# Optimization experiments

Measured on AMD Instinct MI355X. Metric: run time of the kernel, lower is better.

## Reference

```python
import jax, jax.numpy as jnp
import numpy as np

D = 1024      # in_features
H = 768       # hidden_features per routed expert
E = 8         # n_routed_experts
K = 2         # n_activated_experts
NS = 2        # n_shared_experts
ROUTE_SCALE = 1.0


def setup_inputs() -> dict:
    key = jax.random.key(0)
    ks = jax.random.split(key, 6)
    s = 0.02
    return {
        "x": jax.random.normal(ks[0], (2, 1024, D), jnp.float32),
        "gate_w": jax.random.normal(ks[1], (E, D), jnp.float32) * s,
        "W1": jax.random.normal(ks[2], (E, 2 * H, D), jnp.float32) * s,   # expert fc1 (y|gate)
        "W2": jax.random.normal(ks[3], (E, D, H), jnp.float32) * s,       # expert fc2
        "Ws1": jax.random.normal(ks[4], (2 * NS * H, D), jnp.float32) * s,  # shared fc1
        "Ws2": jax.random.normal(ks[5], (D, NS * H), jnp.float32) * s,      # shared fc2
    }


def _gated_mlp(x, w1, w2):
    # GatedMLP: fc1 -> chunk(2) -> y * silu(gate) -> fc2, all bias-free
    h = x @ w1.T
    y, g = jnp.split(h, 2, axis=-1)
    return (y * jax.nn.silu(g)) @ w2.T


def reference(x, gate_w, W1, W2, Ws1, Ws2):
    x_shape = x.shape
    xf = x.reshape(-1, D)                 # [T, D]
    T = xf.shape[0]

    # --- Gate: softmax scores in fp32, top-k routing ---
    scores = jax.nn.softmax((xf @ gate_w.T).astype(jnp.float32), axis=-1)  # [T, E]
    top_vals, top_idx = jax.lax.top_k(scores, K)
    # no bias branch (in_features != 7168): gathered original scores == top_k values
    weights = (top_vals * ROUTE_SCALE).astype(x.dtype)                      # [T, K]

    # Dense per-token/expert combine weights (0 for unselected experts);
    # mathematically identical to the per-expert gather/scatter-add combine.
    w_dense = jnp.zeros((T, E), x.dtype).at[jnp.arange(T)[:, None], top_idx].set(weights)

    # --- Routed experts (stacked GatedMLPs) ---
    h = jnp.einsum('td,ehd->teh', xf, W1)        # [T, E, 2H]
    y, g = jnp.split(h, 2, axis=-1)
    eo = jnp.einsum('teh,edh->ted', y * jax.nn.silu(g), W2)  # [T, E, D]
    z = jnp.einsum('te,ted->td', w_dense, eo)    # weighted combine

    # --- Shared experts ---
    z = z + _gated_mlp(xf, Ws1, Ws2)
    return z.reshape(x_shape)
```

## Files before the change

### kernel.cpp

```cpp
#include <hip/hip_runtime.h>
#include <hip/hip_bf16.h>


typedef short bf16x8 __attribute__((ext_vector_type(8)));
typedef float f32x4 __attribute__((ext_vector_type(4)));

__device__ __forceinline__ unsigned short f2b(float f) {
    __hip_bfloat16 h = __float2bfloat16(f);
    return *reinterpret_cast<unsigned short*>(&h);
}

__device__ __forceinline__ void ldst16(const unsigned short* g, unsigned short* l) {
    __builtin_amdgcn_global_load_lds(
        (const __attribute__((address_space(1))) unsigned int*)g,
        (__attribute__((address_space(3))) unsigned int*)l, 16, 0, 0);
}

__device__ __forceinline__ void cvt8(const float* s, unsigned short* d, int j) {
    const float4* sp = reinterpret_cast<const float4*>(s) + (size_t)j * 2;
    float4 v0 = sp[0], v1 = sp[1];
    union { unsigned short u[8]; uint4 v; } o;
    o.u[0]=f2b(v0.x); o.u[1]=f2b(v0.y); o.u[2]=f2b(v0.z); o.u[3]=f2b(v0.w);
    o.u[4]=f2b(v1.x); o.u[5]=f2b(v1.y); o.u[6]=f2b(v1.z); o.u[7]=f2b(v1.w);
    *(reinterpret_cast<uint4*>(d) + j) = o.v;
}

__global__ __launch_bounds__(256) void k_convgate(const float* __restrict__ x,
                                                  const float* __restrict__ gw,
                                                  const float* __restrict__ W1,
                                                  const float* __restrict__ Ws1,
                                                  unsigned short* __restrict__ xb,
                                                  unsigned short* __restrict__ W1b,
                                                  unsigned short* __restrict__ Ws1b,
                                                  int* __restrict__ tokslot,
                                                  float* __restrict__ wroute,
                                                  int* __restrict__ cnt,
                                                  float* __restrict__ out) {
    __shared__ float red[4][8];
    __shared__ float sc[8];
    const int b = blockIdx.x, tid = threadIdx.x;
    if (b < 7680) {
        int i = b * 256 + tid;
        if (i < 1572864)  cvt8(W1,  W1b,  i);
        else              cvt8(Ws1, Ws1b, i - 1572864);
        return;
    }
    const int t = b - 7680;
    const int lane = tid & 63, w = tid >> 6;

    float4 v = reinterpret_cast<const float4*>(x + (size_t)t * 1024)[tid];
    union { unsigned short u[4]; ushort4 v4; } o;
    o.u[0]=f2b(v.x); o.u[1]=f2b(v.y); o.u[2]=f2b(v.z); o.u[3]=f2b(v.w);
    reinterpret_cast<ushort4*>(xb + (size_t)t * 1024)[tid] = o.v4;

    float p[8];
    for (int e = 0; e < 8; e++) {
        float4 g = reinterpret_cast<const float4*>(gw + (size_t)e * 1024)[tid];
        p[e] = v.x*g.x + v.y*g.y + v.z*g.z + v.w*g.w;
    }
    for (int e = 0; e < 8; e++)
        for (int off = 32; off > 0; off >>= 1) p[e] += __shfl_down(p[e], off, 64);
    if (lane == 0)
        for (int e = 0; e < 8; e++) red[w][e] = p[e];
    __syncthreads();
    if (tid < 8) sc[tid] = red[0][tid] + red[1][tid] + red[2][tid] + red[3][tid];
    __syncthreads();
    if (tid == 0) {
        float m = sc[0];
        for (int e = 1; e < 8; e++) m = fmaxf(m, sc[e]);
        float ex[8], sum = 0.f;
        for (int e = 0; e < 8; e++) { ex[e] = expf(sc[e] - m); sum += ex[e]; }
        float inv = 1.f / sum;
        int i1 = 0;
        for (int e = 1; e < 8; e++) if (sc[e] > sc[i1]) i1 = e;
        int i2 = -1; float s2 = -1e30f;
        for (int e = 0; e < 8; e++) if (e != i1 && sc[e] > s2) { s2 = sc[e]; i2 = e; }
        int p1 = atomicAdd(&cnt[i1 * 16], 1);
        tokslot[i1 * 2048 + p1] = t; wroute[i1 * 2048 + p1] = ex[i1] * inv;
        int p2 = atomicAdd(&cnt[i2 * 16], 1);
        tokslot[i2 * 2048 + p2] = t; wroute[i2 * 2048 + p2] = ex[i2] * inv;
    }
    reinterpret_cast<float4*>(out + (size_t)t * 1024)[tid] = (float4){0.f, 0.f, 0.f, 0.f};
}

__global__ __launch_bounds__(256) void k_fc1w(const unsigned short* __restrict__ xb,
                                              const unsigned short* __restrict__ W1b,
                                              const unsigned short* __restrict__ Ws1b,
                                              const float* __restrict__ W2,
                                              const float* __restrict__ Ws2,
                                              unsigned short* __restrict__ W2b,
                                              unsigned short* __restrict__ Ws2b,
                                              const int* __restrict__ tokslot,
                                              const float* __restrict__ wroute,
                                              const int* __restrict__ cnt,
                                              unsigned short* __restrict__ act_r,
                                              unsigned short* __restrict__ acts) {
    __shared__ alignas(16) unsigned short As[128 * 64];
    __shared__ alignas(16) unsigned short Bs[128 * 64];
    const int tid = threadIdx.x;
    if (blockIdx.x >= 864) {
        int i = (blockIdx.x - 864) * 256 + tid;
        if (i < 786432)  cvt8(W2,  W2b,  i);
        else             cvt8(Ws2, Ws2b, i - 786432);
        return;
    }
    const int lane = tid & 63, w = tid >> 6;
    const int wr = w >> 1, wc = w & 1;
    const int mt = blockIdx.x / 12, ht = blockIdx.x % 12;

    int pre = 0, sel = -1, base = 0;
    for (int ee = 0; ee < 10; ee++) {
        int til = (ee < 8) ? ((cnt[ee * 16] + 127) >> 7) : 16;
        if (sel < 0 && mt < pre + til) { sel = ee; base = pre; }
        pre += til;
    }
    if (sel < 0) return;
    const int e = sel, m0 = (mt - base) * 128, h0 = ht * 64;
    const int Te = (e < 8) ? cnt[e * 16] : 2048;
    const unsigned short* Bp = (e < 8) ? (W1b + (size_t)e * 1536 * 1024)
                                       : (Ws1b + (size_t)(e - 8) * 768 * 1024);
    const int gOff = (e < 8) ? 768 : 1536;

    const int kc = tid & 7;
    int aoff[4], boff[4];
    for (int q = 0; q < 4; q++) {
        int row = q * 32 + (tid >> 3);
        int idx = m0 + row;
        int tk = (e < 8) ? ((idx < Te) ? tokslot[e * 2048 + idx] : 0) : idx;
        aoff[q] = tk * 1024 + ((kc ^ (row & 7)) << 3);
        int grow = (row < 64) ? (h0 + row) : (gOff + h0 + row - 64);
        boff[q] = grow * 1024 + ((kc ^ (row & 7)) << 3);
    }

    f32x4 accy[4][2], accg[4][2];
    for (int i = 0; i < 4; i++)
        for (int j = 0; j < 2; j++) {
            accy[i][j] = (f32x4){0.f, 0.f, 0.f, 0.f};
            accg[i][j] = (f32x4){0.f, 0.f, 0.f, 0.f};
        }

    for (int k0 = 0; k0 < 1024; k0 += 64) {
        for (int q = 0; q < 4; q++) {
            ldst16(xb + aoff[q] + k0, As + (q * 256 + tid) * 8);
            ldst16(Bp + boff[q] + k0, Bs + (q * 256 + tid) * 8);
        }
        __syncthreads();
        for (int kh = 0; kh < 2; kh++) {
            const int cq = kh * 4 + (lane >> 4);
            bf16x8 a[4], by[2], bg[2];
            for (int i = 0; i < 4; i++) {
                int r = 64 * wr + 16 * i + (lane & 15);
                a[i] = *(const bf16x8*)&As[r * 64 + ((cq ^ (r & 7)) << 3)];
            }
            for (int j = 0; j < 2; j++) {
                int ry = 32 * wc + 16 * j + (lane & 15);
                by[j] = *(const bf16x8*)&Bs[ry * 64 + ((cq ^ (ry & 7)) << 3)];
                int rg = 64 + ry;
                bg[j] = *(const bf16x8*)&Bs[rg * 64 + ((cq ^ (rg & 7)) << 3)];
            }
            __builtin_amdgcn_s_setprio(1);
            for (int i = 0; i < 4; i++)
                for (int j = 0; j < 2; j++) {
                    accy[i][j] = __builtin_amdgcn_mfma_f32_16x16x32_bf16(a[i], by[j], accy[i][j], 0, 0, 0);
                    accg[i][j] = __builtin_amdgcn_mfma_f32_16x16x32_bf16(a[i], bg[j], accg[i][j], 0, 0, 0);
                }
            __builtin_amdgcn_s_setprio(0);
        }
        __syncthreads();
    }

    for (int i = 0; i < 4; i++)
        for (int r = 0; r < 4; r++) {
            int irow = m0 + 64 * wr + 16 * i + ((lane >> 4) << 2) + r;
            if (irow >= Te) continue;
            float sw = (e < 8) ? wroute[e * 2048 + irow] : 1.0f;
            unsigned short* dst = (e < 8)
                ? (act_r + ((size_t)e * 2048 + irow) * 768)
                : (acts + (size_t)irow * 1536 + (size_t)(e - 8) * 768);
            for (int j = 0; j < 2; j++) {
                float y = accy[i][j][r], g = accg[i][j][r];
                float sg = g / (1.0f + __expf(-g));
                int col = h0 + 32 * wc + 16 * j + (lane & 15);
                dst[col] = f2b(sw * y * sg);
            }
        }
}

__global__ __launch_bounds__(256) void k_fc2u(const unsigned short* __restrict__ act_r,
                                              const unsigned short* __restrict__ acts,
                                              const unsigned short* __restrict__ W2b,
                                              const unsigned short* __restrict__ Ws2b,
                                              const int* __restrict__ tokslot,
                                              const int* __restrict__ cnt,
                                              float* __restrict__ out) {
    __shared__ alignas(16) unsigned short As[128 * 128];
    __shared__ alignas(16) unsigned short Bs[64 * 128];
    const int tid = threadIdx.x, lane = tid & 63, w = tid >> 6;
    const int wr = w >> 1, wc = w & 1;
    const int mt = blockIdx.x >> 4, nt = blockIdx.x & 15;

    int pre = 0, sel = -1, base = 0;
    for (int ee = 0; ee < 9; ee++) {
        int til = (ee < 8) ? ((cnt[ee * 16] + 127) >> 7) : 16;
        if (sel < 0 && mt < pre + til) { sel = ee; base = pre; }
        pre += til;
    }
    if (sel < 0) return;
    const int e = sel, m0 = (mt - base) * 128, n0 = nt * 64;
    int Te, astride, bstride, K;
    const unsigned short *Ab, *Bb;
    if (e < 8) {
        Te = cnt[e * 16]; K = 768; astride = 768; bstride = 768;
        Ab = act_r + (size_t)e * 2048 * 768;
        Bb = W2b + (size_t)e * 1024 * 768;
    } else {
        Te = 2048; K = 1536; astride = 1536; bstride = 1536;
        Ab = acts;
        Bb = Ws2b;
    }

    const int cp = tid & 15;
    int aoff[8], boff[4];
    for (int q = 0; q < 8; q++) {
        int row = q * 16 + (tid >> 4);
        aoff[q] = (m0 + row) * astride + ((cp ^ (row & 15)) << 3);
    }
    for (int q = 0; q < 4; q++) {
        int row = q * 16 + (tid >> 4);
        boff[q] = (n0 + row) * bstride + ((cp ^ (row & 15)) << 3);
    }

    f32x4 acc[4][2];
    for (int i = 0; i < 4; i++)
        for (int j = 0; j < 2; j++) acc[i][j] = (f32x4){0.f, 0.f, 0.f, 0.f};

    for (int k0 = 0; k0 < K; k0 += 128) {
        for (int q = 0; q < 8; q++) ldst16(Ab + aoff[q] + k0, As + (q * 256 + tid) * 8);
        for (int q = 0; q < 4; q++) ldst16(Bb + boff[q] + k0, Bs + (q * 256 + tid) * 8);
        __syncthreads();
        for (int kh = 0; kh < 4; kh++) {
            const int cq = kh * 4 + (lane >> 4);
            bf16x8 a[4], b[2];
            for (int i = 0; i < 4; i++) {
                int r = 64 * wr + 16 * i + (lane & 15);
                a[i] = *(const bf16x8*)&As[r * 128 + ((cq ^ (r & 15)) << 3)];
            }
            for (int j = 0; j < 2; j++) {
                int rb = 32 * wc + 16 * j + (lane & 15);
                b[j] = *(const bf16x8*)&Bs[rb * 128 + ((cq ^ (rb & 15)) << 3)];
            }
            __builtin_amdgcn_s_setprio(1);
            for (int i = 0; i < 4; i++)
                for (int j = 0; j < 2; j++)
                    acc[i][j] = __builtin_amdgcn_mfma_f32_16x16x32_bf16(a[i], b[j], acc[i][j], 0, 0, 0);
            __builtin_amdgcn_s_setprio(0);
        }
        __syncthreads();
    }

    for (int i = 0; i < 4; i++)
        for (int r = 0; r < 4; r++) {
            int irow = m0 + 64 * wr + 16 * i + ((lane >> 4) << 2) + r;
            if (irow >= Te) continue;
            int t = (e < 8) ? tokslot[e * 2048 + irow] : irow;
            for (int j = 0; j < 2; j++) {
                int col = n0 + 32 * wc + 16 * j + (lane & 15);
                atomicAdd(out + (size_t)t * 1024 + col, acc[i][j][r]);
            }
        }
}

extern "C" void kernel_launch(void* const* d_in, const int* in_sizes, int n_in,
                              void* d_out, int out_size, void* d_ws, size_t ws_size,
                              hipStream_t stream) {
    const float* x   = (const float*)d_in[0];
    const float* gw  = (const float*)d_in[1];
    const float* W1  = (const float*)d_in[2];
    const float* W2  = (const float*)d_in[3];
    const float* Ws1 = (const float*)d_in[4];
    const float* Ws2 = (const float*)d_in[5];
    float* out = (float*)d_out;

    char* ws = (char*)d_ws;
    unsigned short* xb    = (unsigned short*)(ws + 0);
    unsigned short* W1b   = (unsigned short*)(ws + 4194304);
    unsigned short* Ws1b  = (unsigned short*)(ws + 29360128);
    unsigned short* W2b   = (unsigned short*)(ws + 35651584);
    unsigned short* Ws2b  = (unsigned short*)(ws + 48234496);
    unsigned short* act_r = (unsigned short*)(ws + 51380224);
    unsigned short* acts  = (unsigned short*)(ws + 76546048);
    int*            tokslot = (int*)(ws + 82837504);
    float*          wroute  = (float*)(ws + 82903040);
    int*            cnt     = (int*)(ws + 82968576);

    hipMemsetAsync(cnt, 0, 512, stream);
    k_convgate<<<9728, 256, 0, stream>>>(x, gw, W1, Ws1,
                                         xb, W1b, Ws1b,
                                         tokslot, wroute, cnt, out);
    k_fc1w<<<4704, 256, 0, stream>>>(xb, W1b, Ws1b, W2, Ws2, W2b, Ws2b,
                                     tokslot, wroute, cnt, act_r, acts);
    k_fc2u<<<896, 256, 0, stream>>>(act_r, acts, W2b, Ws2b, tokslot, cnt, out);
}
```

Before: 233.9 us.

## Fuse fc1 and fc2 kernels with per-tile readiness counters

Merges the fc1/activation kernel and the fc2 combine kernel into one launch. fc2 blocks spin on agent-scope atomic ready counters set by the matching fc1 row tiles and by the W2 conversion blocks for their expert. The fc2 K-tile shrinks from 128 to 64 so both phases share one 32KB LDS buffer. This removes a kernel boundary and lets fc2 start while other fc1 tiles are still running, but relies on block scheduling order to avoid deadlock and adds spin-wait cost.

```diff
diff --git a/kernel.cpp b/kernel.cpp
--- a/kernel.cpp
+++ b/kernel.cpp
@@ -83,7 +83,7 @@
     reinterpret_cast<float4*>(out + (size_t)t * 1024)[tid] = (float4){0.f, 0.f, 0.f, 0.f};
 }
 
-__global__ __launch_bounds__(256) void k_fc1w(const unsigned short* __restrict__ xb,
+__global__ __launch_bounds__(256) void k_fc12(const unsigned short* __restrict__ xb,
                                               const unsigned short* __restrict__ W1b,
                                               const unsigned short* __restrict__ Ws1b,
                                               const float* __restrict__ W2,
@@ -92,182 +92,218 @@
                                               unsigned short* __restrict__ Ws2b,
                                               const int* __restrict__ tokslot,
                                               const float* __restrict__ wroute,
-                                              const int* __restrict__ cnt,
+                                              int* __restrict__ cntw,
                                               unsigned short* __restrict__ act_r,
-                                              unsigned short* __restrict__ acts) {
-    __shared__ alignas(16) unsigned short As[128 * 64];
-    __shared__ alignas(16) unsigned short Bs[128 * 64];
-    const int tid = threadIdx.x;
-    if (blockIdx.x >= 864) {
-        int i = (blockIdx.x - 864) * 256 + tid;
+                                              unsigned short* __restrict__ acts,
+                                              float* __restrict__ out) {
+    __shared__ alignas(16) unsigned short smem[16384];
+    const int tid = threadIdx.x, bid = blockIdx.x;
+    int* rdy = cntw + 128;
+    int* cvd = cntw + 128 + 2560;
+
+    if (bid >= 864 && bid < 4704) {
+        const int ci = bid - 864;
+        int i = ci * 256 + tid;
         if (i < 786432)  cvt8(W2,  W2b,  i);
         else             cvt8(Ws2, Ws2b, i - 786432);
+        __syncthreads();
+        if (tid == 0) {
+            int e = (ci < 3072) ? (ci / 384) : 8;
+            __hip_atomic_fetch_add(&cvd[e * 16], 1, __ATOMIC_RELEASE,
+                                   __HIP_MEMORY_SCOPE_AGENT);
+        }
         return;
     }
+
     const int lane = tid & 63, w = tid >> 6;
     const int wr = w >> 1, wc = w & 1;
-    const int mt = blockIdx.x / 12, ht = blockIdx.x % 12;
-
-    int pre = 0, sel = -1, base = 0;
-    for (int ee = 0; ee < 10; ee++) {
-        int til = (ee < 8) ? ((cnt[ee * 16] + 127) >> 7) : 16;
-        if (sel < 0 && mt < pre + til) { sel = ee; base = pre; }
-        pre += til;
-    }
-    if (sel < 0) return;
-    const int e = sel, m0 = (mt - base) * 128, h0 = ht * 64;
-    const int Te = (e < 8) ? cnt[e * 16] : 2048;
-    const unsigned short* Bp = (e < 8) ? (W1b + (size_t)e * 1536 * 1024)
-                                       : (Ws1b + (size_t)(e - 8) * 768 * 1024);
-    const int gOff = (e < 8) ? 768 : 1536;
-
-    const int kc = tid & 7;
-    int aoff[4], boff[4];
-    for (int q = 0; q < 4; q++) {
-        int row = q * 32 + (tid >> 3);
-        int idx = m0 + row;
-        int tk = (e < 8) ? ((idx < Te) ? tokslot[e * 2048 + idx] : 0) : idx;
-        aoff[q] = tk * 1024 + ((kc ^ (row & 7)) << 3);
-        int grow = (row < 64) ? (h0 + row) : (gOff + h0 + row - 64);
-        boff[q] = grow * 1024 + ((kc ^ (row & 7)) << 3);
-    }
-
-    f32x4 accy[4][2], accg[4][2];
-    for (int i = 0; i < 4; i++)
-        for (int j = 0; j < 2; j++) {
-            accy[i][j] = (f32x4){0.f, 0.f, 0.f, 0.f};
-            accg[i][j] = (f32x4){0.f, 0.f, 0.f, 0.f};
-        }
-
-    for (int k0 = 0; k0 < 1024; k0 += 64) {
+
+    if (bid < 864) {
+        unsigned short* As = smem;
+        unsigned short* Bs = smem + 8192;
+        const int mt = bid / 12, ht = bid % 12;
+
+        int pre = 0, sel = -1, base = 0;
+        for (int ee = 0; ee < 10; ee++) {
+            int til = (ee < 8) ? ((cntw[ee * 16] + 127) >> 7) : 16;
+            if (sel < 0 && mt < pre + til) { sel = ee; base = pre; }
+            pre += til;
+        }
+        if (sel < 0) return;
+        const int e = sel, m0 = (mt - base) * 128, h0 = ht * 64, mtl = mt - base;
+        const int Te = (e < 8) ? cntw[e * 16] : 2048;
+        const unsigned short* Bp = (e < 8) ? (W1b + (size_t)e * 1536 * 1024)
+                                           : (Ws1b + (size_t)(e - 8) * 768 * 1024);
+        const int gOff = (e < 8) ? 768 : 1536;
+
+        const int kc = tid & 7;
+        int aoff[4], boff[4];
         for (int q = 0; q < 4; q++) {
-            ldst16(xb + aoff[q] + k0, As + (q * 256 + tid) * 8);
-            ldst16(Bp + boff[q] + k0, Bs + (q * 256 + tid) * 8);
-        }
+            int row = q * 32 + (tid >> 3);
+            int idx = m0 + row;
+            int tk = (e < 8) ? ((idx < Te) ? tokslot[e * 2048 + idx] : 0) : idx;
+            aoff[q] = tk * 1024 + ((kc ^ (row & 7)) << 3);
+            int grow = (row < 64) ? (h0 + row) : (gOff + h0 + row - 64);
+            boff[q] = grow * 1024 + ((kc ^ (row & 7)) << 3);
+        }
+
+        f32x4 accy[4][2], accg[4][2];
+        for (int i = 0; i < 4; i++)
+            for (int j = 0; j < 2; j++) {
+                accy[i][j] = (f32x4){0.f, 0.f, 0.f, 0.f};
+                accg[i][j] = (f32x4){0.f, 0.f, 0.f, 0.f};
+            }
+
+        for (int k0 = 0; k0 < 1024; k0 += 64) {
+            for (int q = 0; q < 4; q++) {
+                ldst16(xb + aoff[q] + k0, As + (q * 256 + tid) * 8);
+                ldst16(Bp + boff[q] + k0, Bs + (q * 256 + tid) * 8);
+            }
+            __syncthreads();
+            for (int kh = 0; kh < 2; kh++) {
+                const int cq = kh * 4 + (lane >> 4);
+                bf16x8 a[4], by[2], bg[2];
+                for (int i = 0; i < 4; i++) {
+                    int r = 64 * wr + 16 * i + (lane & 15);
+                    a[i] = *(const bf16x8*)&As[r * 64 + ((cq ^ (r & 7)) << 3)];
+                }
+                for (int j = 0; j < 2; j++) {
+                    int ry = 32 * wc + 16 * j + (lane & 15);
+                    by[j] = *(const bf16x8*)&Bs[ry * 64 + ((cq ^ (ry & 7)) << 3)];
+                    int rg = 64 + ry;
+                    bg[j] = *(const bf16x8*)&Bs[rg * 64 + ((cq ^ (rg & 7)) << 3)];
+                }
+                __builtin_amdgcn_s_setprio(1);
+                for (int i = 0; i < 4; i++)
+                    for (int j = 0; j < 2; j++) {
+                        accy[i][j] = __builtin_amdgcn_mfma_f32_16x16x32_bf16(a[i], by[j], accy[i][j], 0, 0, 0);
+                        accg[i][j] = __builtin_amdgcn_mfma_f32_16x16x32_bf16(a[i], bg[j], accg[i][j], 0, 0, 0);
+                    }
+                __builtin_amdgcn_s_setprio(0);
+            }
+            __syncthreads();
+        }
+
+        for (int i = 0; i < 4; i++)
+            for (int r = 0; r < 4; r++) {
+                int irow = m0 + 64 * wr + 16 * i + ((lane >> 4) << 2) + r;
+                if (irow >= Te) continue;
+                float sw = (e < 8) ? wroute[e * 2048 + irow] : 1.0f;
+                unsigned short* dst = (e < 8)
+                    ? (act_r + ((size_t)e * 2048 + irow) * 768)
+                    : (acts + (size_t)irow * 1536 + (size_t)(e - 8) * 768);
+                for (int j = 0; j < 2; j++) {
+                    float y = accy[i][j][r], g = accg[i][j][r];
+                    float sg = g / (1.0f + __expf(-g));
+                    int col = h0 + 32 * wc + 16 * j + (lane & 15);
+                    dst[col] = f2b(sw * y * sg);
+                }
+            }
         __syncthreads();
-        for (int kh = 0; kh < 2; kh++) {
-            const int cq = kh * 4 + (lane >> 4);
-            bf16x8 a[4], by[2], bg[2];
-            for (int i = 0; i < 4; i++) {
-                int r = 64 * wr + 16 * i + (lane & 15);
-                a[i] = *(const bf16x8*)&As[r * 64 + ((cq ^ (r & 7)) << 3)];
-            }
-            for (int j = 0; j < 2; j++) {
-                int ry = 32 * wc + 16 * j + (lane & 15);
-                by[j] = *(const bf16x8*)&Bs[ry * 64 + ((cq ^ (ry & 7)) << 3)];
-                int rg = 64 + ry;
-                bg[j] = *(const bf16x8*)&Bs[rg * 64 + ((cq ^ (rg & 7)) << 3)];
-            }
-            __builtin_amdgcn_s_setprio(1);
-            for (int i = 0; i < 4; i++)
+        if (tid == 0)
+            __hip_atomic_fetch_add(&rdy[(e * 16 + mtl) * 16], 1, __ATOMIC_RELEASE,
+                                   __HIP_MEMORY_SCOPE_AGENT);
+        return;
+    }
+
+    {
+        unsigned short* As = smem;
+        unsigned short* Bs = smem + 8192;
+        const int fb = bid - 4704;
+        const int mt = fb >> 4, nt = fb & 15;
+
+        int pre = 0, sel = -1, base = 0;
+        for (int ee = 0; ee < 9; ee++) {
+            int til = (ee < 8) ? ((cntw[ee * 16] + 127) >> 7) : 16;
+            if (sel < 0 && mt < pre + til) { sel = ee; base = pre; }
+            pre += til;
+        }
+        if (sel < 0) return;
+        const int e = sel, m0 = (mt - base) * 128, n0 = nt * 64, mtl = mt - base;
+        int Te, astride, bstride, K;
+        const unsigned short *Ab, *Bb;
+        if (e < 8) {
+            Te = cntw[e * 16]; K = 768; astride = 768; bstride = 768;
+            Ab = act_r + (size_t)e * 2048 * 768;
+            Bb = W2b + (size_t)e * 1024 * 768;
+        } else {
+            Te = 2048; K = 1536; astride = 1536; bstride = 1536;
+            Ab = acts;
+            Bb = Ws2b;
+        }
+
+        if (tid == 0) {
+            int spins = 0;
+            if (e < 8) {
+                while (__hip_atomic_load(&rdy[(e * 16 + mtl) * 16], __ATOMIC_ACQUIRE,
+                                         __HIP_MEMORY_SCOPE_AGENT) < 12
+                       && spins < (1 << 22)) { __builtin_amdgcn_s_sleep(8); spins++; }
+                while (__hip_atomic_load(&cvd[e * 16], __ATOMIC_ACQUIRE,
+                                         __HIP_MEMORY_SCOPE_AGENT) < 384
+                       && spins < (1 << 22)) { __builtin_amdgcn_s_sleep(8); spins++; }
+            } else {
+                while ((__hip_atomic_load(&rdy[(128 + mtl) * 16], __ATOMIC_ACQUIRE,
+                                          __HIP_MEMORY_SCOPE_AGENT) < 12 ||
+                        __hip_atomic_load(&rdy[(144 + mtl) * 16], __ATOMIC_ACQUIRE,
+                                          __HIP_MEMORY_SCOPE_AGENT) < 12)
+                       && spins < (1 << 22)) { __builtin_amdgcn_s_sleep(8); spins++; }
+                while (__hip_atomic_load(&cvd[128], __ATOMIC_ACQUIRE,
+                                         __HIP_MEMORY_SCOPE_AGENT) < 768
+                       && spins < (1 << 22)) { __builtin_amdgcn_s_sleep(8); spins++; }
+            }
+        }
+        __syncthreads();
+
+        const int kc = tid & 7;
+        int aoff[4], boff[2];
+        for (int q = 0; q < 4; q++) {
+            int row = q * 32 + (tid >> 3);
+            aoff[q] = (m0 + row) * astride + ((kc ^ (row & 7)) << 3);
+        }
+        for (int q = 0; q < 2; q++) {
+            int row = q * 32 + (tid >> 3);
+            boff[q] = (n0 + row) * bstride + ((kc ^ (row & 7)) << 3);
+        }
+
+        f32x4 acc[4][2];
+        for (int i = 0; i < 4; i++)
+            for (int j = 0; j < 2; j++) acc[i][j] = (f32x4){0.f, 0.f, 0.f, 0.f};
+
+        for (int k0 = 0; k0 < K; k0 += 64) {
+            for (int q = 0; q < 4; q++) ldst16(Ab + aoff[q] + k0, As + (q * 256 + tid) * 8);
+            for (int q = 0; q < 2; q++) ldst16(Bb + boff[q] + k0, Bs + (q * 256 + tid) * 8);
+            __syncthreads();
+            for (int kh = 0; kh < 2; kh++) {
+                const int cq = kh * 4 + (lane >> 4);
+                bf16x8 a[4], b[2];
+                for (int i = 0; i < 4; i++) {
+                    int r = 64 * wr + 16 * i + (lane & 15);
+                    a[i] = *(const bf16x8*)&As[r * 64 + ((cq ^ (r & 7)) << 3)];
+                }
                 for (int j = 0; j < 2; j++) {
-                    accy[i][j] = __builtin_amdgcn_mfma_f32_16x16x32_bf16(a[i], by[j], accy[i][j], 0, 0, 0);
-                    accg[i][j] = __builtin_amdgcn_mfma_f32_16x16x32_bf16(a[i], bg[j], accg[i][j], 0, 0, 0);
-                }
-            __builtin_amdgcn_s_setprio(0);
-        }
-        __syncthreads();
-    }
-
-    for (int i = 0; i < 4; i++)
-        for (int r = 0; r < 4; r++) {
-            int irow = m0 + 64 * wr + 16 * i + ((lane >> 4) << 2) + r;
-            if (irow >= Te) continue;
-            float sw = (e < 8) ? wroute[e * 2048 + irow] : 1.0f;
-            unsigned short* dst = (e < 8)
-                ? (act_r + ((size_t)e * 2048 + irow) * 768)
-                : (acts + (size_t)irow * 1536 + (size_t)(e - 8) * 768);
-            for (int j = 0; j < 2; j++) {
-                float y = accy[i][j][r], g = accg[i][j][r];
-                float sg = g / (1.0f + __expf(-g));
-                int col = h0 + 32 * wc + 16 * j + (lane & 15);
-                dst[col] = f2b(sw * y * sg);
-            }
-        }
-}
-
-__global__ __launch_bounds__(256) void k_fc2u(const unsigned short* __restrict__ act_r,
-                                              const unsigned short* __restrict__ acts,
-                                              const unsigned short* __restrict__ W2b,
-                                              const unsigned short* __restrict__ Ws2b,
-                                              const int* __restrict__ tokslot,
-                                              const int* __restrict__ cnt,
-                                              float* __restrict__ out) {
-    __shared__ alignas(16) unsigned short As[128 * 128];
-    __shared__ alignas(16) unsigned short Bs[64 * 128];
-    const int tid = threadIdx.x, lane = tid & 63, w = tid >> 6;
-    const int wr = w >> 1, wc = w & 1;
-    const int mt = blockIdx.x >> 4, nt = blockIdx.x & 15;
-
-    int pre = 0, sel = -1, base = 0;
-    for (int ee = 0; ee < 9; ee++) {
-        int til = (ee < 8) ? ((cnt[ee * 16] + 127) >> 7) : 16;
-        if (sel < 0 && mt < pre + til) { sel = ee; base = pre; }
-        pre += til;
-    }
-    if (sel < 0) return;
-    const int e = sel, m0 = (mt - base) * 128, n0 = nt * 64;
-    int Te, astride, bstride, K;
-    const unsigned short *Ab, *Bb;
-    if (e < 8) {
-        Te = cnt[e * 16]; K = 768; astride = 768; bstride = 768;
-        Ab = act_r + (size_t)e * 2048 * 768;
-        Bb = W2b + (size_t)e * 1024 * 768;
-    } else {
-        Te = 2048; K = 1536; astride = 1536; bstride = 1536;
-        Ab = acts;
-        Bb = Ws2b;
-    }
-
-    const int cp = tid & 15;
-    int aoff[8], boff[4];
-    for (int q = 0; q < 8; q++) {
-        int row = q * 16 + (tid >> 4);
-        aoff[q] = (m0 + row) * astride + ((cp ^ (row & 15)) << 3);
-    }
-    for (int q = 0; q < 4; q++) {
-        int row = q * 16 + (tid >> 4);
-        boff[q] = (n0 + row) * bstride + ((cp ^ (row & 15)) << 3);
-    }
-
-    f32x4 acc[4][2];
-    for (int i = 0; i < 4; i++)
-        for (int j = 0; j < 2; j++) acc[i][j] = (f32x4){0.f, 0.f, 0.f, 0.f};
-
-    for (int k0 = 0; k0 < K; k0 += 128) {
-        for (int q = 0; q < 8; q++) ldst16(Ab + aoff[q] + k0, As + (q * 256 + tid) * 8);
-        for (int q = 0; q < 4; q++) ldst16(Bb + boff[q] + k0, Bs + (q * 256 + tid) * 8);
-        __syncthreads();
-        for (int kh = 0; kh < 4; kh++) {
-            const int cq = kh * 4 + (lane >> 4);
-            bf16x8 a[4], b[2];
-            for (int i = 0; i < 4; i++) {
-                int r = 64 * wr + 16 * i + (lane & 15);
-                a[i] = *(const bf16x8*)&As[r * 128 + ((cq ^ (r & 15)) << 3)];
-            }
-            for (int j = 0; j < 2; j++) {
-                int rb = 32 * wc + 16 * j + (lane & 15);
-                b[j] = *(const bf16x8*)&Bs[rb * 128 + ((cq ^ (rb & 15)) << 3)];
-            }
-            __builtin_amdgcn_s_setprio(1);
-            for (int i = 0; i < 4; i++)
-                for (int j = 0; j < 2; j++)
-                    acc[i][j] = __builtin_amdgcn_mfma_f32_16x16x32_bf16(a[i], b[j], acc[i][j], 0, 0, 0);
-            __builtin_amdgcn_s_setprio(0);
-        }
-        __syncthreads();
-    }
-
-    for (int i = 0; i < 4; i++)
-        for (int r = 0; r < 4; r++) {
-            int irow = m0 + 64 * wr + 16 * i + ((lane >> 4) << 2) + r;
-            if (irow >= Te) continue;
-            int t = (e < 8) ? tokslot[e * 2048 + irow] : irow;
-            for (int j = 0; j < 2; j++) {
-                int col = n0 + 32 * wc + 16 * j + (lane & 15);
-                atomicAdd(out + (size_t)t * 1024 + col, acc[i][j][r]);
-            }
-        }
+                    int rb = 32 * wc + 16 * j + (lane & 15);
+                    b[j] = *(const bf16x8*)&Bs[rb * 64 + ((cq ^ (rb & 7)) << 3)];
+                }
+                __builtin_amdgcn_s_setprio(1);
+                for (int i = 0; i < 4; i++)
+                    for (int j = 0; j < 2; j++)
+                        acc[i][j] = __builtin_amdgcn_mfma_f32_16x16x32_bf16(a[i], b[j], acc[i][j], 0, 0, 0);
+                __builtin_amdgcn_s_setprio(0);
+            }
+            __syncthreads();
+        }
+
+        for (int i = 0; i < 4; i++)
+            for (int r = 0; r < 4; r++) {
+                int irow = m0 + 64 * wr + 16 * i + ((lane >> 4) << 2) + r;
+                if (irow >= Te) continue;
+                int t = (e < 8) ? tokslot[e * 2048 + irow] : irow;
+                for (int j = 0; j < 2; j++) {
+                    int col = n0 + 32 * wc + 16 * j + (lane & 15);
+                    atomicAdd(out + (size_t)t * 1024 + col, acc[i][j][r]);
+                }
+            }
+    }
 }
 
 extern "C" void kernel_launch(void* const* d_in, const int* in_sizes, int n_in,
@@ -293,11 +329,10 @@
     float*          wroute  = (float*)(ws + 82903040);
     int*            cnt     = (int*)(ws + 82968576);
 
-    hipMemsetAsync(cnt, 0, 512, stream);
+    hipMemsetAsync(cnt, 0, 11328, stream);
     k_convgate<<<9728, 256, 0, stream>>>(x, gw, W1, Ws1,
                                          xb, W1b, Ws1b,
                                          tokslot, wroute, cnt, out);
-    k_fc1w<<<4704, 256, 0, stream>>>(xb, W1b, Ws1b, W2, Ws2, W2b, Ws2b,
-                                     tokslot, wroute, cnt, act_r, acts);
-    k_fc2u<<<896, 256, 0, stream>>>(act_r, acts, W2b, Ws2b, tokslot, cnt, out);
-}
+    k_fc12<<<5600, 256, 0, stream>>>(xb, W1b, Ws1b, W2, Ws2, W2b, Ws2b,
+                                     tokslot, wroute, cnt, act_r, acts, out);
+}
```

Measured after the change: 400.5 us. 71.2% more time.
